# Kernel tuning notes

Hardware: AMD Instinct MI355X
Metric: run time of the kernel (lower is better)

Reference implementation:

```python
import jax, jax.numpy as jnp
import numpy as np

N, K, D = 262144, 1024, 64

def setup_inputs() -> dict:
    key = jax.random.key(0)
    kx, kc = jax.random.split(key)
    x = jax.random.normal(kx, (N, D), dtype=jnp.float32)
    centers = jax.random.normal(kc, (K, D), dtype=jnp.float32)
    return {"x": x, "centers": centers}

def reference(x, centers):
    # centers_norm is precomputed as a buffer in the torch module: (centers**2).sum(-1)
    centers_norm = jnp.sum(centers * centers, axis=-1)           # [K]
    x_norm = jnp.sum(x * x, axis=-1)                             # [N]
    dist = x_norm[..., None] - 2.0 * (x @ centers.T) + centers_norm  # [N,K]
    return jnp.argmin(jnp.abs(dist), axis=-1)                    # [N] int ids
```

## Files before the change

kernel.cpp:

```cpp
#include <hip/hip_runtime.h>
#include <float.h>


#define N_PTS 262144
#define K_CTR 1024
#define DIM   64
#define CTILE 64
#define NTILE (K_CTR / CTILE)
#define OFFC  32.0f
#define TAU_DIST 0.05f

#define WS_CN    0
#define WS_CI    4096
#define WS_HI    8192
#define WS_LO    139264
#define WS_CTR   270336
#define WS_LIST  270592
#define WS_MIN   (270592 + 4 * 65536)

typedef __attribute__((ext_vector_type(8))) short  short8;
typedef __attribute__((ext_vector_type(8))) __bf16 bf16x8;
typedef __attribute__((ext_vector_type(4))) float  f32x4;

union FragU { short8 s; bf16x8 b; unsigned short u[8]; };

static __device__ __forceinline__ unsigned short bfbits(__bf16 h) {
    return __builtin_bit_cast(unsigned short, h);
}

#if defined(__has_builtin)
#if __has_builtin(__builtin_amdgcn_global_load_lds)
#define HAVE_GLD 1
#endif
#endif

#ifdef HAVE_GLD
#define GLD16(gsrc, ldst)                                                      \
    __builtin_amdgcn_global_load_lds(                                          \
        (const __attribute__((address_space(1))) void*)(gsrc),                 \
        (__attribute__((address_space(3))) void*)(ldst), 16, 0, 0)
#endif

__global__ void prep_kernel(const float* __restrict__ centers,
                            float* __restrict__ cn, float* __restrict__ ci,
                            int* __restrict__ counter) {
    int k = blockIdx.x * 256 + threadIdx.x;
    if (k == 0) *counter = 0;
    if (k < K_CTR) {
        const float4* c = reinterpret_cast<const float4*>(centers + (size_t)k * DIM);
        float s0 = 0.f, s1 = 0.f, s2 = 0.f, s3 = 0.f;
#pragma unroll
        for (int j = 0; j < 16; ++j) {
            float4 v = c[j];
            s0 = fmaf(v.x, v.x, s0); s1 = fmaf(v.y, v.y, s1);
            s2 = fmaf(v.z, v.z, s2); s3 = fmaf(v.w, v.w, s3);
        }
        float n = (s0 + s1) + (s2 + s3);
        cn[k] = n;
        ci[k] = fmaf(-0.5f, n, -OFFC);
    }
}

__global__ void split_kernel(const float* __restrict__ centers,
                             unsigned short* __restrict__ hiG,
                             unsigned short* __restrict__ loG) {
    int si = blockIdx.x * 256 + threadIdx.x;
    int lane = si & 63, ks = (si >> 6) & 1, st = (si >> 7) & 3, tile = si >> 9;
    int row = tile * CTILE + st * 16 + (lane & 15);
    int dimb = ks * 32 + ((lane >> 4) & 3) * 8;
    const float* g = centers + (size_t)row * DIM + dimb;
    float4 v0 = *reinterpret_cast<const float4*>(g);
    float4 v1 = *reinterpret_cast<const float4*>(g + 4);
    float vv[8] = {v0.x, v0.y, v0.z, v0.w, v1.x, v1.y, v1.z, v1.w};
    FragU hi, lo;
#pragma unroll
    for (int j = 0; j < 8; ++j) {
        __bf16 h = (__bf16)vv[j];
        hi.u[j] = bfbits(h);
        lo.u[j] = bfbits((__bf16)(vv[j] - (float)h));
    }
    *reinterpret_cast<short8*>(hiG + (size_t)si * 8) = hi.s;
    *reinterpret_cast<short8*>(loG + (size_t)si * 8) = lo.s;
}

__launch_bounds__(256, 2)
__global__ void assign_mfma(const float* __restrict__ x,
                            const unsigned short* __restrict__ hiG,
                            const unsigned short* __restrict__ loG,
                            const float* __restrict__ ci,
                            int* __restrict__ out,
                            int* __restrict__ counter,
                            int* __restrict__ list, int cap) {
    __shared__ __align__(16) unsigned short lh[2 * 512 * 8];
    __shared__ __align__(16) unsigned short ll[2 * 512 * 8];
    __shared__ __align__(16) float ciL[K_CTR];

    const int tid  = threadIdx.x;
    const int wv   = tid >> 6;
    const int lane = tid & 63;
    const int g    = lane >> 4;
    const int lr   = lane & 15;
    const int pbase = blockIdx.x * 256 + wv * 64;

#pragma unroll
    for (int j = 0; j < 4; ++j) ciL[j * 256 + tid] = ci[j * 256 + tid];

    bf16x8 bh[4][2], bl[4][2];
#pragma unroll
    for (int cb = 0; cb < 4; ++cb) {
        const int p = pbase + cb * 16 + lr;
        const float* xr = x + (size_t)p * DIM + g * 8;
        float4 v0 = *reinterpret_cast<const float4*>(xr);
        float4 v1 = *reinterpret_cast<const float4*>(xr + 4);
        float4 v2 = *reinterpret_cast<const float4*>(xr + 32);
        float4 v3 = *reinterpret_cast<const float4*>(xr + 36);
        float vv[16] = {v0.x, v0.y, v0.z, v0.w, v1.x, v1.y, v1.z, v1.w,
                        v2.x, v2.y, v2.z, v2.w, v3.x, v3.y, v3.z, v3.w};
#pragma unroll
        for (int j = 0; j < 16; ++j) {
            __bf16 hb = (__bf16)vv[j];
            bh[cb][j >> 3][j & 7] = hb;
            bl[cb][j >> 3][j & 7] = (__bf16)(vv[j] - (float)hb);
        }
    }

    unsigned int best[4], sec[4];
#pragma unroll
    for (int cb = 0; cb < 4; ++cb) { best[cb] = 0xFFFFFFFFu; sec[cb] = 0xFFFFFFFFu; }

#define STAGE(buf, tile)                                                       \
    do {                                                                       \
        const size_t sb = (size_t)((tile) * 512 + wv * 64 + lane) * 8;         \
        unsigned short* dh = lh + ((buf) * 512 + wv * 64) * 8;                 \
        unsigned short* dl = ll + ((buf) * 512 + wv * 64) * 8;                 \
        GLD16(hiG + sb, dh);                                                   \
        GLD16(hiG + sb + 256 * 8, dh + 256 * 8);                               \
        GLD16(loG + sb, dl);                                                   \
        GLD16(loG + sb + 256 * 8, dl + 256 * 8);                               \
    } while (0)

#ifndef HAVE_GLD
#undef STAGE
#define STAGE(buf, tile)                                                       \
    do {                                                                       \
        const short8* hs = reinterpret_cast<const short8*>(hiG) + (tile) * 512; \
        const short8* ls = reinterpret_cast<const short8*>(loG) + (tile) * 512; \
        short8* hd = reinterpret_cast<short8*>(lh) + (buf) * 512;              \
        short8* ld = reinterpret_cast<short8*>(ll) + (buf) * 512;              \
        hd[tid] = hs[tid]; hd[256 + tid] = hs[256 + tid];                      \
        ld[tid] = ls[tid]; ld[256 + tid] = ls[256 + tid];                      \
    } while (0)
#endif

    STAGE(0, 0);
    __syncthreads();

    int cur = 0;
#pragma unroll 1
    for (int tile = 0; tile < NTILE; ++tile) {
        if (tile < NTILE - 1) STAGE(cur ^ 1, tile + 1);

        const char* lhc = (const char*)lh + cur * 512 * 16 + lane * 16;
        const char* llc = (const char*)ll + cur * 512 * 16 + lane * 16;
        const unsigned int ibt = tile * CTILE + g * 4;
        const float* cib = ciL + tile * CTILE + g * 4;

#pragma unroll
        for (int st = 0; st < CTILE / 16; ++st) {
            FragU ah0, ah1, al0, al1;
            ah0.s = *reinterpret_cast<const short8*>(lhc + st * 2048);
            ah1.s = *reinterpret_cast<const short8*>(lhc + st * 2048 + 1024);
            al0.s = *reinterpret_cast<const short8*>(llc + st * 2048);
            al1.s = *reinterpret_cast<const short8*>(llc + st * 2048 + 1024);
            const f32x4 init4 = *reinterpret_cast<const f32x4*>(cib + st * 16);

            f32x4 acc[4];
            __builtin_amdgcn_s_setprio(1);
#pragma unroll
            for (int cb = 0; cb < 4; ++cb)
                acc[cb] = __builtin_amdgcn_mfma_f32_16x16x32_bf16(ah0.b, bh[cb][0], init4, 0, 0, 0);
#pragma unroll
            for (int cb = 0; cb < 4; ++cb)
                acc[cb] = __builtin_amdgcn_mfma_f32_16x16x32_bf16(ah0.b, bl[cb][0], acc[cb], 0, 0, 0);
#pragma unroll
            for (int cb = 0; cb < 4; ++cb)
                acc[cb] = __builtin_amdgcn_mfma_f32_16x16x32_bf16(al0.b, bh[cb][0], acc[cb], 0, 0, 0);
#pragma unroll
            for (int cb = 0; cb < 4; ++cb)
                acc[cb] = __builtin_amdgcn_mfma_f32_16x16x32_bf16(ah1.b, bh[cb][1], acc[cb], 0, 0, 0);
#pragma unroll
            for (int cb = 0; cb < 4; ++cb)
                acc[cb] = __builtin_amdgcn_mfma_f32_16x16x32_bf16(ah1.b, bl[cb][1], acc[cb], 0, 0, 0);
#pragma unroll
            for (int cb = 0; cb < 4; ++cb)
                acc[cb] = __builtin_amdgcn_mfma_f32_16x16x32_bf16(al1.b, bh[cb][1], acc[cb], 0, 0, 0);
            __builtin_amdgcn_s_setprio(0);

            unsigned int vidx[4];
            vidx[0] = ibt + st * 16;
            vidx[1] = vidx[0] + 1; vidx[2] = vidx[0] + 2; vidx[3] = vidx[0] + 3;

#pragma unroll
            for (int cb = 0; cb < 4; ++cb) {
#pragma unroll
                for (int pr = 0; pr < 2; ++pr) {
                    unsigned int ka = (__float_as_uint(acc[cb][pr * 2 + 0]) & 0xFFFFFC00u) | vidx[pr * 2 + 0];
                    unsigned int kb = (__float_as_uint(acc[cb][pr * 2 + 1]) & 0xFFFFFC00u) | vidx[pr * 2 + 1];
                    unsigned int bo = best[cb], med, bn;
                    asm("v_med3_u32 %0, %1, %2, %3" : "=v"(med) : "v"(ka), "v"(kb), "v"(bo));
                    asm("v_min3_u32 %0, %1, %2, %3" : "=v"(bn)  : "v"(ka), "v"(kb), "v"(bo));
                    best[cb] = bn;
                    sec[cb]  = min(sec[cb], med);
                }
            }
        }

        __syncthreads();
        cur ^= 1;
    }

#pragma unroll
    for (int cb = 0; cb < 4; ++cb) {
        unsigned int b = best[cb], s = sec[cb];
#pragma unroll
        for (int off = 16; off <= 32; off <<= 1) {
            unsigned int ob = __shfl_xor(b, off);
            unsigned int os = __shfl_xor(s, off);
            s = min(min(s, os), max(b, ob));
            b = min(b, ob);
        }
        if (g == 0) {
            const int p = pbase + cb * 16 + lr;
            out[p] = (int)(b & 1023u);
            float bf = __uint_as_float(b & 0xFFFFFC00u);
            float sf = __uint_as_float(s & 0xFFFFFC00u);
            if ((b < 0x80000000u) || (2.f * (bf - sf) < TAU_DIST)) {
                int sl = atomicAdd(counter, 1);
                if (sl < cap) list[sl] = p;
            }
        }
    }
}

__launch_bounds__(256, 2)
__global__ void refine2_kernel(const float* __restrict__ x,
                               const float* __restrict__ centers,
                               const float* __restrict__ cn,
                               const int* __restrict__ list,
                               const int* __restrict__ counter,
                               int* __restrict__ out, int cap) {
    __shared__ float ldsC[64 * 65];
    int cnt = *counter; if (cnt > cap) cnt = cap;
    const int tid  = threadIdx.x;
    const int wv   = tid >> 6;
    const int lane = tid & 63;

#pragma unroll 1
    for (int base = blockIdx.x * 4; base < cnt; base += gridDim.x * 4) {
        const int i = base + wv;
        const bool valid = (i < cnt);
        const int p = valid ? list[i] : 0;

        const float4* xr = reinterpret_cast<const float4*>(x + (size_t)p * DIM);
        float4 xv[16];
        float xn0 = 0.f, xn1 = 0.f, xn2 = 0.f, xn3 = 0.f;
#pragma unroll
        for (int j = 0; j < 16; ++j) {
            float4 v = xr[j]; xv[j] = v;
            xn0 = fmaf(v.x, v.x, xn0); xn1 = fmaf(v.y, v.y, xn1);
            xn2 = fmaf(v.z, v.z, xn2); xn3 = fmaf(v.w, v.w, xn3);
        }
        const float xnv = (xn0 + xn1) + (xn2 + xn3);

        float bestv = 3.4e38f; int bi = 0;
#pragma unroll 1
        for (int t = 0; t < 16; ++t) {
            __syncthreads();
#pragma unroll
            for (int j = 0; j < 16; ++j) {
                int idx = j * 256 + tid;
                int row = idx >> 6, col = idx & 63;
                ldsC[row * 65 + col] = centers[((size_t)t * 64 + row) * DIM + col];
            }
            __syncthreads();
            if (valid) {
                const int k = t * 64 + lane;
                const float* cr = ldsC + lane * 65;
                float a0 = 0.f, a1 = 0.f, a2 = 0.f, a3 = 0.f;
#pragma unroll
                for (int jj = 0; jj < 16; ++jj) {
                    a0 = fmaf(xv[jj].x, cr[jj * 4 + 0], a0);
                    a1 = fmaf(xv[jj].y, cr[jj * 4 + 1], a1);
                    a2 = fmaf(xv[jj].z, cr[jj * 4 + 2], a2);
                    a3 = fmaf(xv[jj].w, cr[jj * 4 + 3], a3);
                }
                float dot  = (a0 + a1) + (a2 + a3);
                float dist = fabsf(fmaf(-2.f, dot, xnv + cn[k]));
                if (dist < bestv) { bestv = dist; bi = k; }
            }
        }
#pragma unroll
        for (int off = 1; off < 64; off <<= 1) {
            float ob = __shfl_xor(bestv, off);
            int   oi = __shfl_xor(bi, off);
            bool take = (ob < bestv) || (ob == bestv && oi < bi);
            bestv = take ? ob : bestv;
            bi    = take ? oi : bi;
        }
        if (valid && lane == 0) out[p] = bi;
    }
}

#define TK 128
__launch_bounds__(256, 4)
__global__ void assign_fp32(const float* __restrict__ x,
                            const float* __restrict__ centers,
                            const float* __restrict__ cn,
                            int* __restrict__ out) {
    __shared__ float ldsC[TK * DIM];
    __shared__ float ldsN[TK];
    const int tid = threadIdx.x;
    const int p = blockIdx.x * 256 + tid;
    const float4* xr = reinterpret_cast<const float4*>(x + (size_t)p * DIM);
    float4 xv[16];
    float xn0 = 0.f, xn1 = 0.f, xn2 = 0.f, xn3 = 0.f;
#pragma unroll
    for (int j = 0; j < 16; ++j) {
        float4 v = xr[j]; xv[j] = v;
        xn0 = fmaf(v.x, v.x, xn0); xn1 = fmaf(v.y, v.y, xn1);
        xn2 = fmaf(v.z, v.z, xn2); xn3 = fmaf(v.w, v.w, xn3);
    }
    const float xn = (xn0 + xn1) + (xn2 + xn3);
    float bestv = 3.4e38f; int best = 0;
#pragma unroll 1
    for (int t = 0; t < K_CTR / TK; ++t) {
        __syncthreads();
        const float4* cg = reinterpret_cast<const float4*>(centers + (size_t)t * TK * DIM);
        float4* cl = reinterpret_cast<float4*>(ldsC);
#pragma unroll
        for (int j = 0; j < (TK * DIM / 4) / 256; ++j)
            cl[j * 256 + tid] = cg[j * 256 + tid];
        if (tid < TK) ldsN[tid] = cn[t * TK + tid];
        __syncthreads();
        for (int k = 0; k < TK; ++k) {
            const float4* cv = reinterpret_cast<const float4*>(ldsC + k * DIM);
            float a0 = 0.f, a1 = 0.f, a2 = 0.f, a3 = 0.f;
#pragma unroll
            for (int j = 0; j < 16; ++j) {
                float4 c4 = cv[j];
                a0 = fmaf(xv[j].x, c4.x, a0); a1 = fmaf(xv[j].y, c4.y, a1);
                a2 = fmaf(xv[j].z, c4.z, a2); a3 = fmaf(xv[j].w, c4.w, a3);
            }
            float dot = (a0 + a1) + (a2 + a3);
            float dist = fabsf(fmaf(-2.f, dot, xn + ldsN[k]));
            if (dist < bestv) { bestv = dist; best = t * TK + k; }
        }
    }
    out[p] = best;
}

extern "C" void kernel_launch(void* const* d_in, const int* in_sizes, int n_in,
                              void* d_out, int out_size, void* d_ws, size_t ws_size,
                              hipStream_t stream) {
    const float* x = (const float*)d_in[0];
    const float* centers = (const float*)d_in[1];
    int* out = (int*)d_out;
    char* ws = (char*)d_ws;
    float* cn = (float*)(ws + WS_CN);
    float* ci = (float*)(ws + WS_CI);
    unsigned short* hiG = (unsigned short*)(ws + WS_HI);
    unsigned short* loG = (unsigned short*)(ws + WS_LO);
    int* counter = (int*)(ws + WS_CTR);
    int* list = (int*)(ws + WS_LIST);

    if (ws_size >= WS_MIN) {
        size_t avail = (ws_size - WS_LIST) / sizeof(int);
        int cap = (int)(avail < (size_t)N_PTS ? avail : (size_t)N_PTS);
        prep_kernel<<<4, 256, 0, stream>>>(centers, cn, ci, counter);
        split_kernel<<<32, 256, 0, stream>>>(centers, hiG, loG);
        assign_mfma<<<N_PTS / 256, 256, 0, stream>>>(x, hiG, loG, ci, out, counter, list, cap);
        refine2_kernel<<<1024, 256, 0, stream>>>(x, centers, cn, list, counter, out, cap);
    } else {
        prep_kernel<<<4, 256, 0, stream>>>(centers, cn, ci, counter);
        assign_fp32<<<N_PTS / 256, 256, 0, stream>>>(x, centers, cn, out);
    }
}
```

Measured before the change: 118.1 us.

## Load center fragments directly from global into registers, dropping LDS staging

Replaces the double-buffered LDS staging of the bf16 hi/lo center fragments (global_load_lds plus a __syncthreads per tile) with direct per-wave global loads into registers, software-pipelined two 16-center tiles ahead. The center layout is simplified to 16-row chunks. This removes the per-tile block barriers and the LDS traffic. In exchange each of the four waves reads the same fragments from L1/L2 independently, and global load latency now has to be hidden by the register prefetch.

```diff
diff --git a/kernel.cpp b/kernel.cpp
--- a/kernel.cpp
+++ b/kernel.cpp
@@ -5,8 +5,6 @@
 #define N_PTS 262144
 #define K_CTR 1024
 #define DIM   64
-#define CTILE 64
-#define NTILE (K_CTR / CTILE)
 #define OFFC  32.0f
 #define TAU_DIST 0.05f
 
@@ -27,19 +25,6 @@
 static __device__ __forceinline__ unsigned short bfbits(__bf16 h) {
     return __builtin_bit_cast(unsigned short, h);
 }
-
-#if defined(__has_builtin)
-#if __has_builtin(__builtin_amdgcn_global_load_lds)
-#define HAVE_GLD 1
-#endif
-#endif
-
-#ifdef HAVE_GLD
-#define GLD16(gsrc, ldst)                                                      \
-    __builtin_amdgcn_global_load_lds(                                          \
-        (const __attribute__((address_space(1))) void*)(gsrc),                 \
-        (__attribute__((address_space(3))) void*)(ldst), 16, 0, 0)
-#endif
 
 __global__ void prep_kernel(const float* __restrict__ centers,
                             float* __restrict__ cn, float* __restrict__ ci,
@@ -65,8 +50,8 @@
                              unsigned short* __restrict__ hiG,
                              unsigned short* __restrict__ loG) {
     int si = blockIdx.x * 256 + threadIdx.x;
-    int lane = si & 63, ks = (si >> 6) & 1, st = (si >> 7) & 3, tile = si >> 9;
-    int row = tile * CTILE + st * 16 + (lane & 15);
+    int lane = si & 63, ks = (si >> 6) & 1, ct = si >> 7;
+    int row = ct * 16 + (lane & 15);
     int dimb = ks * 32 + ((lane >> 4) & 3) * 8;
     const float* g = centers + (size_t)row * DIM + dimb;
     float4 v0 = *reinterpret_cast<const float4*>(g);
@@ -91,8 +76,6 @@
                             int* __restrict__ out,
                             int* __restrict__ counter,
                             int* __restrict__ list, int cap) {
-    __shared__ __align__(16) unsigned short lh[2 * 512 * 8];
-    __shared__ __align__(16) unsigned short ll[2 * 512 * 8];
     __shared__ __align__(16) float ciL[K_CTR];
 
     const int tid  = threadIdx.x;
@@ -128,95 +111,70 @@
 #pragma unroll
     for (int cb = 0; cb < 4; ++cb) { best[cb] = 0xFFFFFFFFu; sec[cb] = 0xFFFFFFFFu; }
 
-#define STAGE(buf, tile)                                                       \
+    __syncthreads();
+
+    const short8* hp = reinterpret_cast<const short8*>(hiG) + lane;
+    const short8* lp = reinterpret_cast<const short8*>(loG) + lane;
+
+#define LOADA(A0, A1, A2, A3, ct)                                              \
     do {                                                                       \
-        const size_t sb = (size_t)((tile) * 512 + wv * 64 + lane) * 8;         \
-        unsigned short* dh = lh + ((buf) * 512 + wv * 64) * 8;                 \
-        unsigned short* dl = ll + ((buf) * 512 + wv * 64) * 8;                 \
-        GLD16(hiG + sb, dh);                                                   \
-        GLD16(hiG + sb + 256 * 8, dh + 256 * 8);                               \
-        GLD16(loG + sb, dl);                                                   \
-        GLD16(loG + sb + 256 * 8, dl + 256 * 8);                               \
+        (A0).s = hp[(ct) * 128];      (A1).s = hp[(ct) * 128 + 64];            \
+        (A2).s = lp[(ct) * 128];      (A3).s = lp[(ct) * 128 + 64];            \
     } while (0)
 
-#ifndef HAVE_GLD
-#undef STAGE
-#define STAGE(buf, tile)                                                       \
-    do {                                                                       \
-        const short8* hs = reinterpret_cast<const short8*>(hiG) + (tile) * 512; \
-        const short8* ls = reinterpret_cast<const short8*>(loG) + (tile) * 512; \
-        short8* hd = reinterpret_cast<short8*>(lh) + (buf) * 512;              \
-        short8* ld = reinterpret_cast<short8*>(ll) + (buf) * 512;              \
-        hd[tid] = hs[tid]; hd[256 + tid] = hs[256 + tid];                      \
-        ld[tid] = ls[tid]; ld[256 + tid] = ls[256 + tid];                      \
-    } while (0)
-#endif
-
-    STAGE(0, 0);
-    __syncthreads();
-
-    int cur = 0;
+    auto compute = [&](const FragU& A0, const FragU& A1,
+                       const FragU& A2, const FragU& A3, int ct) {
+        const f32x4 init4 = *reinterpret_cast<const f32x4*>(ciL + ct * 16 + g * 4);
+        f32x4 acc[4];
+        __builtin_amdgcn_s_setprio(1);
+#pragma unroll
+        for (int cb = 0; cb < 4; ++cb)
+            acc[cb] = __builtin_amdgcn_mfma_f32_16x16x32_bf16(A0.b, bh[cb][0], init4, 0, 0, 0);
+#pragma unroll
+        for (int cb = 0; cb < 4; ++cb)
+            acc[cb] = __builtin_amdgcn_mfma_f32_16x16x32_bf16(A0.b, bl[cb][0], acc[cb], 0, 0, 0);
+#pragma unroll
+        for (int cb = 0; cb < 4; ++cb)
+            acc[cb] = __builtin_amdgcn_mfma_f32_16x16x32_bf16(A2.b, bh[cb][0], acc[cb], 0, 0, 0);
+#pragma unroll
+        for (int cb = 0; cb < 4; ++cb)
+            acc[cb] = __builtin_amdgcn_mfma_f32_16x16x32_bf16(A1.b, bh[cb][1], acc[cb], 0, 0, 0);
+#pragma unroll
+        for (int cb = 0; cb < 4; ++cb)
+            acc[cb] = __builtin_amdgcn_mfma_f32_16x16x32_bf16(A1.b, bl[cb][1], acc[cb], 0, 0, 0);
+#pragma unroll
+        for (int cb = 0; cb < 4; ++cb)
+            acc[cb] = __builtin_amdgcn_mfma_f32_16x16x32_bf16(A3.b, bh[cb][1], acc[cb], 0, 0, 0);
+        __builtin_amdgcn_s_setprio(0);
+
+        unsigned int vidx[4];
+        vidx[0] = (unsigned int)(ct * 16 + g * 4);
+        vidx[1] = vidx[0] + 1; vidx[2] = vidx[0] + 2; vidx[3] = vidx[0] + 3;
+
+#pragma unroll
+        for (int cb = 0; cb < 4; ++cb) {
+#pragma unroll
+            for (int pr = 0; pr < 2; ++pr) {
+                unsigned int ka = (__float_as_uint(acc[cb][pr * 2 + 0]) & 0xFFFFFC00u) | vidx[pr * 2 + 0];
+                unsigned int kb = (__float_as_uint(acc[cb][pr * 2 + 1]) & 0xFFFFFC00u) | vidx[pr * 2 + 1];
+                unsigned int bo = best[cb], med, bn;
+                asm("v_med3_u32 %0, %1, %2, %3" : "=v"(med) : "v"(ka), "v"(kb), "v"(bo));
+                asm("v_min3_u32 %0, %1, %2, %3" : "=v"(bn)  : "v"(ka), "v"(kb), "v"(bo));
+                best[cb] = bn;
+                sec[cb]  = min(sec[cb], med);
+            }
+        }
+    };
+
+    FragU pa0, pa1, pa2, pa3, pb0, pb1, pb2, pb3;
+    LOADA(pa0, pa1, pa2, pa3, 0);
+
 #pragma unroll 1
-    for (int tile = 0; tile < NTILE; ++tile) {
-        if (tile < NTILE - 1) STAGE(cur ^ 1, tile + 1);
-
-        const char* lhc = (const char*)lh + cur * 512 * 16 + lane * 16;
-        const char* llc = (const char*)ll + cur * 512 * 16 + lane * 16;
-        const unsigned int ibt = tile * CTILE + g * 4;
-        const float* cib = ciL + tile * CTILE + g * 4;
-
-#pragma unroll
-        for (int st = 0; st < CTILE / 16; ++st) {
-            FragU ah0, ah1, al0, al1;
-            ah0.s = *reinterpret_cast<const short8*>(lhc + st * 2048);
-            ah1.s = *reinterpret_cast<const short8*>(lhc + st * 2048 + 1024);
-            al0.s = *reinterpret_cast<const short8*>(llc + st * 2048);
-            al1.s = *reinterpret_cast<const short8*>(llc + st * 2048 + 1024);
-            const f32x4 init4 = *reinterpret_cast<const f32x4*>(cib + st * 16);
-
-            f32x4 acc[4];
-            __builtin_amdgcn_s_setprio(1);
-#pragma unroll
-            for (int cb = 0; cb < 4; ++cb)
-                acc[cb] = __builtin_amdgcn_mfma_f32_16x16x32_bf16(ah0.b, bh[cb][0], init4, 0, 0, 0);
-#pragma unroll
-            for (int cb = 0; cb < 4; ++cb)
-                acc[cb] = __builtin_amdgcn_mfma_f32_16x16x32_bf16(ah0.b, bl[cb][0], acc[cb], 0, 0, 0);
-#pragma unroll
-            for (int cb = 0; cb < 4; ++cb)
-                acc[cb] = __builtin_amdgcn_mfma_f32_16x16x32_bf16(al0.b, bh[cb][0], acc[cb], 0, 0, 0);
-#pragma unroll
-            for (int cb = 0; cb < 4; ++cb)
-                acc[cb] = __builtin_amdgcn_mfma_f32_16x16x32_bf16(ah1.b, bh[cb][1], acc[cb], 0, 0, 0);
-#pragma unroll
-            for (int cb = 0; cb < 4; ++cb)
-                acc[cb] = __builtin_amdgcn_mfma_f32_16x16x32_bf16(ah1.b, bl[cb][1], acc[cb], 0, 0, 0);
-#pragma unroll
-            for (int cb = 0; cb < 4; ++cb)
-                acc[cb] = __builtin_amdgcn_mfma_f32_16x16x32_bf16(al1.b, bh[cb][1], acc[cb], 0, 0, 0);
-            __builtin_amdgcn_s_setprio(0);
-
-            unsigned int vidx[4];
-            vidx[0] = ibt + st * 16;
-            vidx[1] = vidx[0] + 1; vidx[2] = vidx[0] + 2; vidx[3] = vidx[0] + 3;
-
-#pragma unroll
-            for (int cb = 0; cb < 4; ++cb) {
-#pragma unroll
-                for (int pr = 0; pr < 2; ++pr) {
-                    unsigned int ka = (__float_as_uint(acc[cb][pr * 2 + 0]) & 0xFFFFFC00u) | vidx[pr * 2 + 0];
-                    unsigned int kb = (__float_as_uint(acc[cb][pr * 2 + 1]) & 0xFFFFFC00u) | vidx[pr * 2 + 1];
-                    unsigned int bo = best[cb], med, bn;
-                    asm("v_med3_u32 %0, %1, %2, %3" : "=v"(med) : "v"(ka), "v"(kb), "v"(bo));
-                    asm("v_min3_u32 %0, %1, %2, %3" : "=v"(bn)  : "v"(ka), "v"(kb), "v"(bo));
-                    best[cb] = bn;
-                    sec[cb]  = min(sec[cb], med);
-                }
-            }
-        }
-
-        __syncthreads();
-        cur ^= 1;
+    for (int ct = 0; ct < 64; ct += 2) {
+        LOADA(pb0, pb1, pb2, pb3, ct + 1);
+        compute(pa0, pa1, pa2, pa3, ct);
+        if (ct + 2 < 64) LOADA(pa0, pa1, pa2, pa3, ct + 2);
+        compute(pb0, pb1, pb2, pb3, ct + 1);
     }
 
 #pragma unroll
@@ -240,6 +198,7 @@
             }
         }
     }
+#undef LOADA
 }
 
 __launch_bounds__(256, 2)
```

After: 134.2 us. 1.14x slower.

## Stage center tiles per wave to drop block barriers and stagger tile order

Applied to the files above, without the earlier changes.

Each wave now loads its own 16-center tile into a private double buffer. It waits only on its own vmcnt instead of a block-wide __syncthreads every tile. Waves and blocks also start at staggered tile offsets so global reads of the split centers are spread out. The risks are more loop iterations with less MFMA work each, 4x redundant center loads per block, and correctness that depends on the async-load wait counts and the absence of a cross-lane LDS barrier.

```diff
diff --git a/kernel.cpp b/kernel.cpp
--- a/kernel.cpp
+++ b/kernel.cpp
@@ -5,7 +5,7 @@
 #define N_PTS 262144
 #define K_CTR 1024
 #define DIM   64
-#define CTILE 64
+#define CTILE 16
 #define NTILE (K_CTR / CTILE)
 #define OFFC  32.0f
 #define TAU_DIST 0.05f
@@ -65,8 +65,8 @@
                              unsigned short* __restrict__ hiG,
                              unsigned short* __restrict__ loG) {
     int si = blockIdx.x * 256 + threadIdx.x;
-    int lane = si & 63, ks = (si >> 6) & 1, st = (si >> 7) & 3, tile = si >> 9;
-    int row = tile * CTILE + st * 16 + (lane & 15);
+    int lane = si & 63, ks = (si >> 6) & 1, g16 = si >> 7;
+    int row = g16 * 16 + (lane & 15);
     int dimb = ks * 32 + ((lane >> 4) & 3) * 8;
     const float* g = centers + (size_t)row * DIM + dimb;
     float4 v0 = *reinterpret_cast<const float4*>(g);
@@ -91,8 +91,8 @@
                             int* __restrict__ out,
                             int* __restrict__ counter,
                             int* __restrict__ list, int cap) {
-    __shared__ __align__(16) unsigned short lh[2 * 512 * 8];
-    __shared__ __align__(16) unsigned short ll[2 * 512 * 8];
+    __shared__ __align__(16) unsigned short lh[4 * 2 * 128 * 8];
+    __shared__ __align__(16) unsigned short ll[4 * 2 * 128 * 8];
     __shared__ __align__(16) float ciL[K_CTR];
 
     const int tid  = threadIdx.x;
@@ -101,6 +101,7 @@
     const int g    = lane >> 4;
     const int lr   = lane & 15;
     const int pbase = blockIdx.x * 256 + wv * 64;
+    const int wbase = wv * 256;
 
 #pragma unroll
     for (int j = 0; j < 4; ++j) ciL[j * 256 + tid] = ci[j * 256 + tid];
@@ -130,92 +131,95 @@
 
 #define STAGE(buf, tile)                                                       \
     do {                                                                       \
-        const size_t sb = (size_t)((tile) * 512 + wv * 64 + lane) * 8;         \
-        unsigned short* dh = lh + ((buf) * 512 + wv * 64) * 8;                 \
-        unsigned short* dl = ll + ((buf) * 512 + wv * 64) * 8;                 \
+        const size_t sb = (size_t)((tile) * 128 + lane) * 8;                   \
+        unsigned short* dh = lh + (size_t)(wbase + (buf) * 128) * 8;           \
+        unsigned short* dl = ll + (size_t)(wbase + (buf) * 128) * 8;           \
         GLD16(hiG + sb, dh);                                                   \
-        GLD16(hiG + sb + 256 * 8, dh + 256 * 8);                               \
+        GLD16(hiG + sb + 64 * 8, dh + 64 * 8);                                 \
         GLD16(loG + sb, dl);                                                   \
-        GLD16(loG + sb + 256 * 8, dl + 256 * 8);                               \
+        GLD16(loG + sb + 64 * 8, dl + 64 * 8);                                 \
     } while (0)
 
 #ifndef HAVE_GLD
 #undef STAGE
 #define STAGE(buf, tile)                                                       \
     do {                                                                       \
-        const short8* hs = reinterpret_cast<const short8*>(hiG) + (tile) * 512; \
-        const short8* ls = reinterpret_cast<const short8*>(loG) + (tile) * 512; \
-        short8* hd = reinterpret_cast<short8*>(lh) + (buf) * 512;              \
-        short8* ld = reinterpret_cast<short8*>(ll) + (buf) * 512;              \
-        hd[tid] = hs[tid]; hd[256 + tid] = hs[256 + tid];                      \
-        ld[tid] = ls[tid]; ld[256 + tid] = ls[256 + tid];                      \
+        const short8* hs = reinterpret_cast<const short8*>(hiG) + (tile) * 128; \
+        const short8* ls = reinterpret_cast<const short8*>(loG) + (tile) * 128; \
+        short8* hd = reinterpret_cast<short8*>(lh) + wbase + (buf) * 128;      \
+        short8* ld = reinterpret_cast<short8*>(ll) + wbase + (buf) * 128;      \
+        hd[lane] = hs[lane]; hd[64 + lane] = hs[64 + lane];                    \
+        ld[lane] = ls[lane]; ld[64 + lane] = ls[64 + lane];                    \
     } while (0)
 #endif
 
-    STAGE(0, 0);
+    const int tstart = ((blockIdx.x & 63) + wv * 16) & 63;
+
+    STAGE(0, tstart);
     __syncthreads();
 
     int cur = 0;
 #pragma unroll 1
-    for (int tile = 0; tile < NTILE; ++tile) {
-        if (tile < NTILE - 1) STAGE(cur ^ 1, tile + 1);
-
-        const char* lhc = (const char*)lh + cur * 512 * 16 + lane * 16;
-        const char* llc = (const char*)ll + cur * 512 * 16 + lane * 16;
-        const unsigned int ibt = tile * CTILE + g * 4;
-        const float* cib = ciL + tile * CTILE + g * 4;
-
-#pragma unroll
-        for (int st = 0; st < CTILE / 16; ++st) {
-            FragU ah0, ah1, al0, al1;
-            ah0.s = *reinterpret_cast<const short8*>(lhc + st * 2048);
-            ah1.s = *reinterpret_cast<const short8*>(lhc + st * 2048 + 1024);
-            al0.s = *reinterpret_cast<const short8*>(llc + st * 2048);
-            al1.s = *reinterpret_cast<const short8*>(llc + st * 2048 + 1024);
-            const f32x4 init4 = *reinterpret_cast<const f32x4*>(cib + st * 16);
-
-            f32x4 acc[4];
-            __builtin_amdgcn_s_setprio(1);
-#pragma unroll
-            for (int cb = 0; cb < 4; ++cb)
-                acc[cb] = __builtin_amdgcn_mfma_f32_16x16x32_bf16(ah0.b, bh[cb][0], init4, 0, 0, 0);
-#pragma unroll
-            for (int cb = 0; cb < 4; ++cb)
-                acc[cb] = __builtin_amdgcn_mfma_f32_16x16x32_bf16(ah0.b, bl[cb][0], acc[cb], 0, 0, 0);
-#pragma unroll
-            for (int cb = 0; cb < 4; ++cb)
-                acc[cb] = __builtin_amdgcn_mfma_f32_16x16x32_bf16(al0.b, bh[cb][0], acc[cb], 0, 0, 0);
-#pragma unroll
-            for (int cb = 0; cb < 4; ++cb)
-                acc[cb] = __builtin_amdgcn_mfma_f32_16x16x32_bf16(ah1.b, bh[cb][1], acc[cb], 0, 0, 0);
-#pragma unroll
-            for (int cb = 0; cb < 4; ++cb)
-                acc[cb] = __builtin_amdgcn_mfma_f32_16x16x32_bf16(ah1.b, bl[cb][1], acc[cb], 0, 0, 0);
-#pragma unroll
-            for (int cb = 0; cb < 4; ++cb)
-                acc[cb] = __builtin_amdgcn_mfma_f32_16x16x32_bf16(al1.b, bh[cb][1], acc[cb], 0, 0, 0);
-            __builtin_amdgcn_s_setprio(0);
-
-            unsigned int vidx[4];
-            vidx[0] = ibt + st * 16;
-            vidx[1] = vidx[0] + 1; vidx[2] = vidx[0] + 2; vidx[3] = vidx[0] + 3;
-
-#pragma unroll
-            for (int cb = 0; cb < 4; ++cb) {
-#pragma unroll
-                for (int pr = 0; pr < 2; ++pr) {
-                    unsigned int ka = (__float_as_uint(acc[cb][pr * 2 + 0]) & 0xFFFFFC00u) | vidx[pr * 2 + 0];
-                    unsigned int kb = (__float_as_uint(acc[cb][pr * 2 + 1]) & 0xFFFFFC00u) | vidx[pr * 2 + 1];
-                    unsigned int bo = best[cb], med, bn;
-                    asm("v_med3_u32 %0, %1, %2, %3" : "=v"(med) : "v"(ka), "v"(kb), "v"(bo));
-                    asm("v_min3_u32 %0, %1, %2, %3" : "=v"(bn)  : "v"(ka), "v"(kb), "v"(bo));
-                    best[cb] = bn;
-                    sec[cb]  = min(sec[cb], med);
-                }
-            }
-        }
-
-        __syncthreads();
+    for (int i = 0; i < NTILE; ++i) {
+        const int t = (tstart + i) & (NTILE - 1);
+        if (i < NTILE - 1) {
+            const int tn = (t + 1) & (NTILE - 1);
+            STAGE(cur ^ 1, tn);
+            asm volatile("s_waitcnt vmcnt(4)" ::: "memory");
+        } else {
+            asm volatile("s_waitcnt vmcnt(0)" ::: "memory");
+        }
+
+        const char* lhc = (const char*)lh + (size_t)(wbase + cur * 128) * 16 + lane * 16;
+        const char* llc = (const char*)ll + (size_t)(wbase + cur * 128) * 16 + lane * 16;
+
+        FragU ah0, ah1, al0, al1;
+        ah0.s = *reinterpret_cast<const short8*>(lhc);
+        ah1.s = *reinterpret_cast<const short8*>(lhc + 1024);
+        al0.s = *reinterpret_cast<const short8*>(llc);
+        al1.s = *reinterpret_cast<const short8*>(llc + 1024);
+        const f32x4 init4 = *reinterpret_cast<const f32x4*>(ciL + t * CTILE + g * 4);
+
+        f32x4 acc[4];
+        __builtin_amdgcn_s_setprio(1);
+#pragma unroll
+        for (int cb = 0; cb < 4; ++cb)
+            acc[cb] = __builtin_amdgcn_mfma_f32_16x16x32_bf16(ah0.b, bh[cb][0], init4, 0, 0, 0);
+#pragma unroll
+        for (int cb = 0; cb < 4; ++cb)
+            acc[cb] = __builtin_amdgcn_mfma_f32_16x16x32_bf16(ah0.b, bl[cb][0], acc[cb], 0, 0, 0);
+#pragma unroll
+        for (int cb = 0; cb < 4; ++cb)
+            acc[cb] = __builtin_amdgcn_mfma_f32_16x16x32_bf16(al0.b, bh[cb][0], acc[cb], 0, 0, 0);
+#pragma unroll
+        for (int cb = 0; cb < 4; ++cb)
+            acc[cb] = __builtin_amdgcn_mfma_f32_16x16x32_bf16(ah1.b, bh[cb][1], acc[cb], 0, 0, 0);
+#pragma unroll
+        for (int cb = 0; cb < 4; ++cb)
+            acc[cb] = __builtin_amdgcn_mfma_f32_16x16x32_bf16(ah1.b, bl[cb][1], acc[cb], 0, 0, 0);
+#pragma unroll
+        for (int cb = 0; cb < 4; ++cb)
+            acc[cb] = __builtin_amdgcn_mfma_f32_16x16x32_bf16(al1.b, bh[cb][1], acc[cb], 0, 0, 0);
+        __builtin_amdgcn_s_setprio(0);
+
+        unsigned int vidx[4];
+        vidx[0] = (unsigned int)(t * CTILE + g * 4);
+        vidx[1] = vidx[0] + 1; vidx[2] = vidx[0] + 2; vidx[3] = vidx[0] + 3;
+
+#pragma unroll
+        for (int cb = 0; cb < 4; ++cb) {
+#pragma unroll
+            for (int pr = 0; pr < 2; ++pr) {
+                unsigned int ka = (__float_as_uint(acc[cb][pr * 2 + 0]) & 0xFFFFFC00u) | vidx[pr * 2 + 0];
+                unsigned int kb = (__float_as_uint(acc[cb][pr * 2 + 1]) & 0xFFFFFC00u) | vidx[pr * 2 + 1];
+                unsigned int bo = best[cb], med, bn;
+                asm("v_med3_u32 %0, %1, %2, %3" : "=v"(med) : "v"(ka), "v"(kb), "v"(bo));
+                asm("v_min3_u32 %0, %1, %2, %3" : "=v"(bn)  : "v"(ka), "v"(kb), "v"(bo));
+                best[cb] = bn;
+                sec[cb]  = min(sec[cb], med);
+            }
+        }
+
         cur ^= 1;
     }
 
```

Measured after the change: 131.3 us. +11.2%, slower.

## Software-pipeline argmin epilogue one step behind MFMA and interleave with sched barriers

Applied to the files above, without the earlier changes.

Each sub-tile's min/second-min update now works on the previous step's MFMA results, so the VALU comparisons can overlap the current step's MFMA chain. The setup adds a -inf sentinel accumulator and a drain step after the loop. sched_group_barrier hints interleave groups of 4 MFMAs with 12 VALU ops, and the s_setprio calls and inline med3/min3 asm are replaced by plain min/max. This holds more accumulator registers live, which can lower occupancy, and the compiler may not produce the schedule the hints ask for.

```diff
diff --git a/kernel.cpp b/kernel.cpp
--- a/kernel.cpp
+++ b/kernel.cpp
@@ -32,6 +32,9 @@
 #if __has_builtin(__builtin_amdgcn_global_load_lds)
 #define HAVE_GLD 1
 #endif
+#if __has_builtin(__builtin_amdgcn_sched_group_barrier)
+#define HAVE_SGB 1
+#endif
 #endif
 
 #ifdef HAVE_GLD
@@ -39,6 +42,19 @@
     __builtin_amdgcn_global_load_lds(                                          \
         (const __attribute__((address_space(1))) void*)(gsrc),                 \
         (__attribute__((address_space(3))) void*)(ldst), 16, 0, 0)
+#endif
+
+#ifdef HAVE_SGB
+#define SGB_ST()                                                               \
+    do {                                                                       \
+        _Pragma("unroll")                                                      \
+        for (int i2 = 0; i2 < 6; ++i2) {                                       \
+            __builtin_amdgcn_sched_group_barrier(0x8, 4, 0);                   \
+            __builtin_amdgcn_sched_group_barrier(0x2, 12, 0);                  \
+        }                                                                      \
+    } while (0)
+#else
+#define SGB_ST() do {} while (0)
 #endif
 
 __global__ void prep_kernel(const float* __restrict__ centers,
@@ -152,8 +168,30 @@
     } while (0)
 #endif
 
+#define EPILOGUE(AP, V0)                                                       \
+    do {                                                                       \
+        _Pragma("unroll")                                                      \
+        for (int cb = 0; cb < 4; ++cb) {                                       \
+            _Pragma("unroll")                                                  \
+            for (int pr = 0; pr < 2; ++pr) {                                   \
+                unsigned int ka = (__float_as_uint((AP)[cb][pr * 2 + 0]) & 0xFFFFFC00u) | ((V0) + pr * 2 + 0); \
+                unsigned int kb = (__float_as_uint((AP)[cb][pr * 2 + 1]) & 0xFFFFFC00u) | ((V0) + pr * 2 + 1); \
+                unsigned int lo = min(ka, kb), hi = max(ka, kb);               \
+                sec[cb]  = min(sec[cb], max(lo, min(hi, best[cb])));           \
+                best[cb] = min(best[cb], lo);                                  \
+            }                                                                  \
+        }                                                                      \
+    } while (0)
+
     STAGE(0, 0);
     __syncthreads();
+
+    f32x4 accP[4];
+#pragma unroll
+    for (int cb = 0; cb < 4; ++cb)
+        accP[cb] = (f32x4){-__builtin_inff(), -__builtin_inff(),
+                           -__builtin_inff(), -__builtin_inff()};
+    unsigned int vidxP = 0;
 
     int cur = 0;
 #pragma unroll 1
@@ -175,7 +213,6 @@
             const f32x4 init4 = *reinterpret_cast<const f32x4*>(cib + st * 16);
 
             f32x4 acc[4];
-            __builtin_amdgcn_s_setprio(1);
 #pragma unroll
             for (int cb = 0; cb < 4; ++cb)
                 acc[cb] = __builtin_amdgcn_mfma_f32_16x16x32_bf16(ah0.b, bh[cb][0], init4, 0, 0, 0);
@@ -194,30 +231,21 @@
 #pragma unroll
             for (int cb = 0; cb < 4; ++cb)
                 acc[cb] = __builtin_amdgcn_mfma_f32_16x16x32_bf16(al1.b, bh[cb][1], acc[cb], 0, 0, 0);
-            __builtin_amdgcn_s_setprio(0);
-
-            unsigned int vidx[4];
-            vidx[0] = ibt + st * 16;
-            vidx[1] = vidx[0] + 1; vidx[2] = vidx[0] + 2; vidx[3] = vidx[0] + 3;
-
-#pragma unroll
-            for (int cb = 0; cb < 4; ++cb) {
-#pragma unroll
-                for (int pr = 0; pr < 2; ++pr) {
-                    unsigned int ka = (__float_as_uint(acc[cb][pr * 2 + 0]) & 0xFFFFFC00u) | vidx[pr * 2 + 0];
-                    unsigned int kb = (__float_as_uint(acc[cb][pr * 2 + 1]) & 0xFFFFFC00u) | vidx[pr * 2 + 1];
-                    unsigned int bo = best[cb], med, bn;
-                    asm("v_med3_u32 %0, %1, %2, %3" : "=v"(med) : "v"(ka), "v"(kb), "v"(bo));
-                    asm("v_min3_u32 %0, %1, %2, %3" : "=v"(bn)  : "v"(ka), "v"(kb), "v"(bo));
-                    best[cb] = bn;
-                    sec[cb]  = min(sec[cb], med);
-                }
-            }
+
+            EPILOGUE(accP, vidxP);
+
+#pragma unroll
+            for (int cb = 0; cb < 4; ++cb) accP[cb] = acc[cb];
+            vidxP = ibt + st * 16;
+
+            SGB_ST();
         }
 
         __syncthreads();
         cur ^= 1;
     }
+
+    EPILOGUE(accP, vidxP);
 
 #pragma unroll
     for (int cb = 0; cb < 4; ++cb) {
```

After: 125.8 us. +6.5%, slower.
